# Kernel tuning notes

Hardware: AMD Instinct MI355X
Metric: run time of the kernel (lower is better)

The kernel has to match this reference:

```python
import jax, jax.numpy as jnp
import numpy as np

B, S, D, H = 16, 577, 768, 12  # batch, seq (24*24+1 cls), hidden, heads
WH, WW = 24, 24
HEAD = D // H
NUM_REL = (2 * WH - 1) * (2 * WW - 1) + 3  # 2212


def make_rel_pos_index(wh, ww):
    # mirrors TFData2VecVisionRelativePositionBias.get_position_index
    xx, yy = np.meshgrid(np.arange(wh), np.arange(ww))  # 'xy' indexing like tf.meshgrid
    coords = np.stack([yy, xx], axis=0).reshape(2, -1)  # [2, wh*ww]
    rel = coords[:, :, None] - coords[:, None, :]       # [2, N, N]
    rel = rel.transpose(1, 2, 0)                        # [N, N, 2]
    rx = (rel[:, :, 0] + wh - 1) * (2 * ww - 1)
    ry = rel[:, :, 1] + ww - 1
    idx = rx + ry                                       # [N, N]
    n = idx.shape[0]
    top = np.full((1, n), NUM_REL - 3, dtype=idx.dtype)
    left = np.full((n, 1), NUM_REL - 2, dtype=idx.dtype)
    corner = np.full((1, 1), NUM_REL - 1, dtype=idx.dtype)
    idx = np.concatenate([top, idx], axis=0)
    idx = np.concatenate([np.concatenate([corner, left], axis=0), idx], axis=1)
    return idx.astype(np.int32)  # [N+1, N+1]


def setup_inputs() -> dict:
    key = jax.random.key(0)
    ks = jax.random.split(key, 6)
    scale = 0.02
    return {
        "hidden_states": jax.random.normal(ks[0], (B, S, D), jnp.float32),
        "Wq": jax.random.normal(ks[1], (D, D), jnp.float32) * scale,
        "bq": jnp.zeros((D,), jnp.float32),
        "Wk": jax.random.normal(ks[2], (D, D), jnp.float32) * scale,
        "Wv": jax.random.normal(ks[3], (D, D), jnp.float32) * scale,
        "bv": jnp.zeros((D,), jnp.float32),
        "rel_pos_bias_table": jax.random.normal(ks[4], (NUM_REL, H), jnp.float32) * scale,
        "rel_pos_index": jnp.asarray(make_rel_pos_index(WH, WW)),
    }


def reference(hidden_states, Wq, bq, Wk, Wv, bv, rel_pos_bias_table, rel_pos_index):
    b, s, _ = hidden_states.shape
    q = (hidden_states @ Wq + bq).reshape(b, s, H, HEAD).transpose(0, 2, 1, 3)
    k = (hidden_states @ Wk).reshape(b, s, H, HEAD).transpose(0, 2, 1, 3)
    v = (hidden_states @ Wv + bv).reshape(b, s, H, HEAD).transpose(0, 2, 1, 3)
    scores = jnp.einsum("bhqd,bhkd->bhqk", q, k) / jnp.sqrt(jnp.float32(HEAD))
    # gathered relative position bias: [S, S, H] -> [H, S, S]
    bias = rel_pos_bias_table[rel_pos_index].transpose(2, 0, 1)
    scores = scores + bias[None]
    probs = jax.nn.softmax(scores, axis=-1)
    out = jnp.einsum("bhqk,bhkd->bhqd", probs, v)
    out = out.transpose(0, 2, 1, 3).reshape(b, s, D)
    return out
```

## Files before the change

### kernel.cpp

```cpp
#include <hip/hip_runtime.h>
#include <hip/hip_bf16.h>


typedef __attribute__((ext_vector_type(8))) short bf16x8;
typedef __attribute__((ext_vector_type(4))) float f32x4;
typedef unsigned short u16;

#define SEQ 577
#define MTOT 9232
#define QKV_STRIDE 7090176
#define VT_PITCH 640
#define B_PITCH 640

static __device__ __forceinline__ u16 f2bf(float x) {
  unsigned int u = __float_as_uint(x);
  u = (u + 0x7FFFu + ((u >> 16) & 1u)) >> 16;
  return (u16)u;
}
static __device__ __forceinline__ float bf2f(u16 v) {
  return __uint_as_float(((unsigned int)v) << 16);
}

static __device__ __forceinline__ void gload_lds16(const void* g, void* l) {
  __builtin_amdgcn_global_load_lds(
      (const __attribute__((address_space(1))) unsigned int*)g,
      (__attribute__((address_space(3))) unsigned int*)l, 16, 0, 0);
}

__global__ __launch_bounds__(256) void prep(
    const float* __restrict__ Wq, const float* __restrict__ Wk,
    const float* __restrict__ Wv, const float* __restrict__ X,
    u16* __restrict__ WT, u16* __restrict__ Xb) {
  const int bid = blockIdx.x;
  if (bid < 1728) {
    __shared__ float t[32][33];
    const int z = bid / 576;
    const int rem = bid - z * 576;
    const int kx = rem % 24, ny = rem / 24;
    const float* W = (z == 0) ? Wq : (z == 1) ? Wk : Wv;
    int x = threadIdx.x & 31;
    int y = threadIdx.x >> 5;
    int k0 = kx * 32;
    int n0 = ny * 32;
#pragma unroll
    for (int i = 0; i < 4; ++i)
      t[y + i * 8][x] = W[(size_t)(k0 + y + i * 8) * 768 + n0 + x];
    __syncthreads();
    u16* o = WT + (size_t)z * 589824;
#pragma unroll
    for (int i = 0; i < 4; ++i)
      o[(size_t)(n0 + y + i * 8) * 768 + k0 + x] = f2bf(t[x][y + i * 8]);
  } else {
    size_t i = ((size_t)(bid - 1728) * 256 + threadIdx.x) * 8;
    if (i >= (size_t)MTOT * 768) return;
    const float4* xp = (const float4*)(X + i);
    float4 a = xp[0], b = xp[1];
    u16 pk[8] = {f2bf(a.x), f2bf(a.y), f2bf(a.z), f2bf(a.w),
                 f2bf(b.x), f2bf(b.y), f2bf(b.z), f2bf(b.w)};
    *(int4*)(Xb + i) = *(const int4*)pk;
  }
}

__global__ __launch_bounds__(256) void prep2(
    const u16* __restrict__ v,
    u16* __restrict__ vT,
    const float* __restrict__ table, const int* __restrict__ idx,
    u16* __restrict__ biasm) {
  const int bid = blockIdx.x;
  const int tid = threadIdx.x;
  if (bid < 960) {
    const int tile = bid % 5;
    const int bh = bid / 5;
    const int b = bh / 12, h = bh % 12;
    __shared__ u16 T[128][64];
    const int s0 = tile * 128;
    const u16* vp = v + (size_t)b * SEQ * 768 + h * 64;
#pragma unroll
    for (int it = 0; it < 4; ++it) {
      int c = tid + it * 256;
      int r = c >> 3, ko = (c & 7) << 3;
      int gs = s0 + r;
      int4 val = make_int4(0, 0, 0, 0);
      if (gs < SEQ) val = *(const int4*)(vp + (size_t)gs * 768 + ko);
      *(int4*)&T[r][ko ^ (((r >> 3) & 7) << 3)] = val;
    }
    __syncthreads();
    u16* op = vT + (size_t)bh * 64 * VT_PITCH;
#pragma unroll
    for (int it = 0; it < 4; ++it) {
      int c = tid + it * 256;
      int d = c >> 4, so = (c & 15) << 3;
      u16 tmp[8];
#pragma unroll
      for (int j = 0; j < 8; ++j) {
        int rr = so + j;
        tmp[j] = T[rr][d ^ (((rr >> 3) & 7) << 3)];
      }
      *(int4*)(op + (size_t)d * VT_PITCH + s0 + so) = *(const int4*)tmp;
    }
  } else {
    const int r = bid - 960;
    const int q = r % 577;
    const int h = r / 577;
    for (int k = tid; k < B_PITCH; k += 256) {
      u16 vv = 0;
      if (k < SEQ) vv = f2bf(table[idx[q * SEQ + k] * 12 + h]);
      biasm[((size_t)h * SEQ + q) * B_PITCH + k] = vv;
    }
  }
}

__global__ __launch_bounds__(256) void qkv_gemm(
    const u16* __restrict__ Xb,
    const u16* __restrict__ WT,
    const float* __restrict__ bq, const float* __restrict__ bv,
    u16* __restrict__ qkv) {
  const int bid = blockIdx.x;
  const int xcd = bid & 7;
  const int local = bid >> 3;
  const int mp = (local / 18) * 8 + xcd;
  if (mp >= 73) return;
  const int nw = local % 18;
  const int widx = nw % 3;
  const int m0 = mp * 128;
  const int n0 = (nw / 3) * 128;

  const int tid = threadIdx.x;
  const int lane = tid & 63;
  const int w = tid >> 6;
  const int wm = (w >> 1) * 64;
  const int wn = (w & 1) * 64;
  const int quad = lane >> 4;
  const int l15 = lane & 15;

  __shared__ u16 SH[2][2][128][32];

  const u16* Wp = WT + (size_t)widx * 589824;

  const int srow = w * 32 + (lane >> 2);
  const int scol = (lane & 3) * 8;

  int r0 = m0 + srow;
  int r1 = r0 + 16;
  if (r0 > MTOT - 1) r0 = MTOT - 1;
  if (r1 > MTOT - 1) r1 = MTOT - 1;
  const u16* a0 = Xb + (size_t)r0 * 768 + scol;
  const u16* a1 = Xb + (size_t)r1 * 768 + scol;
  const u16* b0 = Wp + (size_t)(n0 + srow) * 768 + scol;
  const u16* b1 = Wp + (size_t)(n0 + srow + 16) * 768 + scol;

  f32x4 acc[4][4];
#pragma unroll
  for (int i = 0; i < 4; ++i)
#pragma unroll
    for (int j = 0; j < 4; ++j) acc[i][j] = (f32x4){0.f, 0.f, 0.f, 0.f};

  gload_lds16(a0, &SH[0][0][w * 32][0]);
  gload_lds16(a1, &SH[0][0][w * 32 + 16][0]);
  gload_lds16(b0, &SH[0][1][w * 32][0]);
  gload_lds16(b1, &SH[0][1][w * 32 + 16][0]);
  __syncthreads();

  for (int kt = 0; kt < 24; ++kt) {
    const int cur = kt & 1;
    if (kt < 23) {
      const int k1 = (kt + 1) * 32;
      const int nb = cur ^ 1;
      gload_lds16(a0 + k1, &SH[nb][0][w * 32][0]);
      gload_lds16(a1 + k1, &SH[nb][0][w * 32 + 16][0]);
      gload_lds16(b0 + k1, &SH[nb][1][w * 32][0]);
      gload_lds16(b1 + k1, &SH[nb][1][w * 32 + 16][0]);
    }
    bf16x8 af[4], bfv[4];
#pragma unroll
    for (int i = 0; i < 4; ++i)
      af[i] = *(const bf16x8*)(&SH[cur][0][wm + i * 16 + l15][quad * 8]);
#pragma unroll
    for (int i = 0; i < 4; ++i)
      bfv[i] = *(const bf16x8*)(&SH[cur][1][wn + i * 16 + l15][quad * 8]);
#pragma unroll
    for (int mt = 0; mt < 4; ++mt)
#pragma unroll
      for (int nt = 0; nt < 4; ++nt)
        acc[mt][nt] = __builtin_amdgcn_mfma_f32_16x16x32_bf16(af[mt], bfv[nt],
                                                              acc[mt][nt], 0, 0, 0);
    __syncthreads();
  }

  const float scale = (widx == 0) ? 0.125f : 1.0f;
  u16* ob = qkv + (size_t)widx * QKV_STRIDE;
  float biasv[4];
#pragma unroll
  for (int nt = 0; nt < 4; ++nt) {
    int n = n0 + wn + nt * 16 + l15;
    biasv[nt] = (widx == 0) ? bq[n] * 0.125f : (widx == 2) ? bv[n] : 0.f;
  }
  u16* S = &SH[0][0][0][0];
#pragma unroll
  for (int half = 0; half < 2; ++half) {
    if ((w >> 1) == half) {
#pragma unroll
      for (int mt = 0; mt < 4; ++mt)
#pragma unroll
        for (int nt = 0; nt < 4; ++nt)
#pragma unroll
          for (int r = 0; r < 4; ++r) {
            int rowl = mt * 16 + quad * 4 + r;
            int col = wn + nt * 16 + l15;
            int cs = (col + quad * 32) & 127;
            S[rowl * 128 + cs] = f2bf(acc[mt][nt][r] * scale + biasv[nt]);
          }
    }
    __syncthreads();
#pragma unroll
    for (int it = 0; it < 4; ++it) {
      int c = tid + it * 256;
      int rowl = c >> 4, ch = c & 15;
      int m = m0 + half * 64 + rowl;
      if (m < MTOT) {
        int cs = (ch * 8 + ((rowl >> 2) & 3) * 32) & 127;
        *(int4*)(ob + (size_t)m * 768 + n0 + ch * 8) = *(const int4*)&S[rowl * 128 + cs];
      }
    }
    __syncthreads();
  }
}

__global__ __launch_bounds__(512) void attn(
    const u16* __restrict__ qk, const u16* __restrict__ vT,
    const u16* __restrict__ biasm, float* __restrict__ out) {
  const int bh = blockIdx.x;
  const int qt = blockIdx.y;
  const int b = bh / 12, h = bh - b * 12;
  const int tid = threadIdx.x;
  const int lane = tid & 63;
  const int w = tid >> 6;
  const int quad = lane >> 4;
  const int l15 = lane & 15;

  const u16* qp = qk + (size_t)b * SEQ * 768 + h * 64;
  const u16* kp = qp + (size_t)QKV_STRIDE;
  const u16* vtp = vT + (size_t)bh * 64 * VT_PITCH;
  const u16* bp = biasm + (size_t)h * SEQ * B_PITCH;

  __shared__ u16 Ks[64][72];
  __shared__ u16 VTs[64][72];
  __shared__ u16 Ps[8][16][72];

  const int qrow0 = qt * 128 + w * 16;

  bf16x8 qf[2];
  {
    int row = qrow0 + l15;
    if (row > 576) row = 576;
    qf[0] = *(const bf16x8*)(qp + (size_t)row * 768 + quad * 8);
    qf[1] = *(const bf16x8*)(qp + (size_t)row * 768 + 32 + quad * 8);
  }
  int brow[4];
#pragma unroll
  for (int r = 0; r < 4; ++r) {
    int rr = qrow0 + quad * 4 + r;
    if (rr > 576) rr = 576;
    brow[r] = rr;
  }

  float lacc[4] = {0.f, 0.f, 0.f, 0.f};
  f32x4 O[4];
#pragma unroll
  for (int dt = 0; dt < 4; ++dt) O[dt] = (f32x4){0.f, 0.f, 0.f, 0.f};

  for (int kt = 0; kt < 10; ++kt) {
    const int kbase = kt * 64;
    u16 bb[4][4];
#pragma unroll
    for (int nt = 0; nt < 4; ++nt)
#pragma unroll
      for (int r = 0; r < 4; ++r)
        bb[nt][r] = bp[(size_t)brow[r] * B_PITCH + kbase + nt * 16 + l15];

    {
      int rr = tid >> 3, ko = (tid & 7) << 3;
      int gk = kbase + rr;
      int4 kvv = make_int4(0, 0, 0, 0);
      if (gk < SEQ) kvv = *(const int4*)(kp + (size_t)gk * 768 + ko);
      *(int4*)&Ks[rr][ko] = kvv;
      *(int4*)&VTs[rr][ko] = *(const int4*)(vtp + (size_t)rr * VT_PITCH + kbase + ko);
    }
    __syncthreads();

    f32x4 s[4];
#pragma unroll
    for (int nt = 0; nt < 4; ++nt) {
      f32x4 z = (f32x4){bf2f(bb[nt][0]), bf2f(bb[nt][1]),
                        bf2f(bb[nt][2]), bf2f(bb[nt][3])};
      bf16x8 kf0 = *(const bf16x8*)(&Ks[nt * 16 + l15][quad * 8]);
      bf16x8 kf1 = *(const bf16x8*)(&Ks[nt * 16 + l15][32 + quad * 8]);
      z = __builtin_amdgcn_mfma_f32_16x16x32_bf16(qf[0], kf0, z, 0, 0, 0);
      z = __builtin_amdgcn_mfma_f32_16x16x32_bf16(qf[1], kf1, z, 0, 0, 0);
      s[nt] = z;
    }

    const bool full = (kbase + 64 <= SEQ);
#pragma unroll
    for (int nt = 0; nt < 4; ++nt) {
#pragma unroll
      for (int r = 0; r < 4; ++r) {
        float p = __expf(s[nt][r]);
        unsigned int u = __float_as_uint(p);
        float pt = __uint_as_float(u & 0xFFFF0000u);
        if (full) lacc[r] += pt;
        else lacc[r] += ((kbase + nt * 16 + l15) < SEQ) ? pt : 0.f;
        Ps[w][quad * 4 + r][((nt ^ quad) << 4) + l15] = (u16)(u >> 16);
      }
    }

#pragma unroll
    for (int ks = 0; ks < 2; ++ks) {
      int cc = (ks * 32 + quad * 8) ^ ((l15 >> 2) << 4);
      bf16x8 pf = *(const bf16x8*)(&Ps[w][l15][cc]);
#pragma unroll
      for (int dt = 0; dt < 4; ++dt) {
        bf16x8 vf = *(const bf16x8*)(&VTs[dt * 16 + l15][ks * 32 + quad * 8]);
        O[dt] = __builtin_amdgcn_mfma_f32_16x16x32_bf16(pf, vf, O[dt], 0, 0, 0);
      }
    }
    __syncthreads();
  }

#pragma unroll
  for (int r = 0; r < 4; ++r) {
    float l = lacc[r];
    l += __shfl_xor(l, 1);
    l += __shfl_xor(l, 2);
    l += __shfl_xor(l, 4);
    l += __shfl_xor(l, 8);
    int row = qrow0 + quad * 4 + r;
    if (row < SEQ) {
      float inv = 1.f / l;
#pragma unroll
      for (int dt = 0; dt < 4; ++dt)
        out[((size_t)(b * SEQ + row)) * 768 + h * 64 + dt * 16 + l15] = O[dt][r] * inv;
    }
  }
}

extern "C" void kernel_launch(void* const* d_in, const int* in_sizes, int n_in,
                              void* d_out, int out_size, void* d_ws, size_t ws_size,
                              hipStream_t stream) {
  const float* hs = (const float*)d_in[0];
  const float* Wq = (const float*)d_in[1];
  const float* bq = (const float*)d_in[2];
  const float* Wk = (const float*)d_in[3];
  const float* Wv = (const float*)d_in[4];
  const float* bv = (const float*)d_in[5];
  const float* table = (const float*)d_in[6];
  const int* idx = (const int*)d_in[7];
  float* out = (float*)d_out;

  char* ws = (char*)d_ws;
  u16* qkv = (u16*)ws;
  u16* WT = (u16*)(ws + 42541056);
  u16* Xb = (u16*)(ws + 46080000);
  u16* vT = (u16*)(ws + 42541056);
  u16* biasm = (u16*)(ws + 58269696);

  hipLaunchKernelGGL(prep, dim3(5190), dim3(256), 0, stream, Wq, Wk, Wv, hs, WT, Xb);
  hipLaunchKernelGGL(qkv_gemm, dim3(1440), dim3(256), 0, stream, Xb, WT, bq, bv, qkv);
  hipLaunchKernelGGL(prep2, dim3(7884), dim3(256), 0, stream,
                     qkv + 2 * (size_t)QKV_STRIDE, vT, table, idx, biasm);
  hipLaunchKernelGGL(attn, dim3(192, 5), dim3(512), 0, stream, qkv, vT, biasm, out);
}
```

Measured before the change: 208.5 us.

## Enlarge QKV GEMM tiles with triple-buffered LDS and prefetch attention operands

The QKV GEMM moves from 128x128 tiles with 256 threads and double buffering to 256x384 tiles with 512 threads. It adds triple-buffered direct-to-LDS loads, XOR-swizzled LDS layout, explicit waitcnt/barrier scheduling and MFMA priority raising. The aim is more operand reuse per block and less LDS and global traffic per FLOP. The relative-position bias matrix is stored transposed (key-major), so each lane loads four consecutive query biases as one short4 instead of four scalar loads. The attention loop also register-prefetches the next K, V^T and bias tiles to overlap global loads with compute. The cost is higher register pressure and only 240 GEMM blocks, which may underfill the GPU.

After: 223.6 us. +7.3%, slower.

```diff
diff --git a/kernel.cpp b/kernel.cpp
--- a/kernel.cpp
+++ b/kernel.cpp
@@ -10,7 +10,8 @@
 #define MTOT 9232
 #define QKV_STRIDE 7090176
 #define VT_PITCH 640
-#define B_PITCH 640
+#define BT_K 584
+#define BT_Q 632
 
 static __device__ __forceinline__ u16 f2bf(float x) {
   unsigned int u = __float_as_uint(x);
@@ -65,7 +66,7 @@
     const u16* __restrict__ v,
     u16* __restrict__ vT,
     const float* __restrict__ table, const int* __restrict__ idx,
-    u16* __restrict__ biasm) {
+    u16* __restrict__ biasT) {
   const int bid = blockIdx.x;
   const int tid = threadIdx.x;
   if (bid < 960) {
@@ -100,126 +101,166 @@
     }
   } else {
     const int r = bid - 960;
-    const int q = r % 577;
-    const int h = r / 577;
-    for (int k = tid; k < B_PITCH; k += 256) {
+    const int k = r % BT_K;
+    const int h = r / BT_K;
+    u16* op = biasT + ((size_t)h * BT_K + k) * BT_Q;
+    for (int q = tid; q < BT_Q; q += 256) {
       u16 vv = 0;
-      if (k < SEQ) vv = f2bf(table[idx[q * SEQ + k] * 12 + h]);
-      biasm[((size_t)h * SEQ + q) * B_PITCH + k] = vv;
-    }
-  }
-}
-
-__global__ __launch_bounds__(256) void qkv_gemm(
+      if (q < SEQ && k < SEQ) vv = f2bf(table[idx[q * SEQ + k] * 12 + h]);
+      op[q] = vv;
+    }
+  }
+}
+
+#define G_STAGE_A(BS, KT, U)                                                   \
+  gload_lds16(aptr[(U)] + (KT) * 32, &SAB[(BS)][((U) * 128 + w16) * 32])
+#define G_STAGE_B(BS, KT, U)                                                   \
+  gload_lds16(bptr + (size_t)(U) * 128 * 768 + (KT) * 32,                      \
+              &SAB[(BS)][8192 + ((U) * 128 + w16) * 32])
+
+__global__ __launch_bounds__(512, 2) void qkv_gemm(
     const u16* __restrict__ Xb,
     const u16* __restrict__ WT,
     const float* __restrict__ bq, const float* __restrict__ bv,
     u16* __restrict__ qkv) {
   const int bid = blockIdx.x;
-  const int xcd = bid & 7;
-  const int local = bid >> 3;
-  const int mp = (local / 18) * 8 + xcd;
-  if (mp >= 73) return;
-  const int nw = local % 18;
-  const int widx = nw % 3;
-  const int m0 = mp * 128;
-  const int n0 = (nw / 3) * 128;
+  const int x = bid & 7;
+  const int l = bid >> 3;
+  const int mt = x + 8 * (l / 6);
+  if (mt >= 37) return;
+  const int nt = l % 6;
+  const int m0 = mt * 256;
+  const int widx = nt >> 1;
+  const int nb = (nt & 1) * 384;
 
   const int tid = threadIdx.x;
   const int lane = tid & 63;
   const int w = tid >> 6;
-  const int wm = (w >> 1) * 64;
-  const int wn = (w & 1) * 64;
+  const int wm2 = w >> 2;
+  const int wn = w & 3;
   const int quad = lane >> 4;
   const int l15 = lane & 15;
-
-  __shared__ u16 SH[2][2][128][32];
-
-  const u16* Wp = WT + (size_t)widx * 589824;
-
-  const int srow = w * 32 + (lane >> 2);
-  const int scol = (lane & 3) * 8;
-
-  int r0 = m0 + srow;
-  int r1 = r0 + 16;
-  if (r0 > MTOT - 1) r0 = MTOT - 1;
-  if (r1 > MTOT - 1) r1 = MTOT - 1;
-  const u16* a0 = Xb + (size_t)r0 * 768 + scol;
-  const u16* a1 = Xb + (size_t)r1 * 768 + scol;
-  const u16* b0 = Wp + (size_t)(n0 + srow) * 768 + scol;
-  const u16* b1 = Wp + (size_t)(n0 + srow + 16) * 768 + scol;
-
-  f32x4 acc[4][4];
-#pragma unroll
-  for (int i = 0; i < 4; ++i)
-#pragma unroll
-    for (int j = 0; j < 4; ++j) acc[i][j] = (f32x4){0.f, 0.f, 0.f, 0.f};
-
-  gload_lds16(a0, &SH[0][0][w * 32][0]);
-  gload_lds16(a1, &SH[0][0][w * 32 + 16][0]);
-  gload_lds16(b0, &SH[0][1][w * 32][0]);
-  gload_lds16(b1, &SH[0][1][w * 32 + 16][0]);
-  __syncthreads();
-
-  for (int kt = 0; kt < 24; ++kt) {
-    const int cur = kt & 1;
-    if (kt < 23) {
-      const int k1 = (kt + 1) * 32;
-      const int nb = cur ^ 1;
-      gload_lds16(a0 + k1, &SH[nb][0][w * 32][0]);
-      gload_lds16(a1 + k1, &SH[nb][0][w * 32 + 16][0]);
-      gload_lds16(b0 + k1, &SH[nb][1][w * 32][0]);
-      gload_lds16(b1 + k1, &SH[nb][1][w * 32 + 16][0]);
-    }
-    bf16x8 af[4], bfv[4];
+  const int w16 = w * 16;
+
+  __shared__ u16 SAB[3][20480];
+
+  const int srow = w16 + (lane >> 2);
+  const int ce8 = (((lane & 3) ^ ((lane >> 3) & 3))) * 8;
+  const u16* aptr[2];
+#pragma unroll
+  for (int u = 0; u < 2; ++u) {
+    int rr = m0 + u * 128 + srow;
+    if (rr > MTOT - 1) rr = MTOT - 1;
+    aptr[u] = Xb + (size_t)rr * 768 + ce8;
+  }
+  const u16* bptr =
+      WT + (size_t)widx * 589824 + (size_t)(nb + srow) * 768 + ce8;
+
+  const int ca8 = (quad ^ ((l15 >> 1) & 3)) * 8;
+
+  f32x4 acc[8][6];
+#pragma unroll
+  for (int i = 0; i < 8; ++i)
+#pragma unroll
+    for (int j = 0; j < 6; ++j) acc[i][j] = (f32x4){0.f, 0.f, 0.f, 0.f};
+  bf16x8 af[4], bfr[6];
+
+  G_STAGE_A(0, 0, 0); G_STAGE_A(0, 0, 1);
+  G_STAGE_B(0, 0, 0); G_STAGE_B(0, 0, 1); G_STAGE_B(0, 0, 2);
+  G_STAGE_A(1, 1, 0); G_STAGE_A(1, 1, 1);
+  G_STAGE_B(1, 1, 0); G_STAGE_B(1, 1, 1); G_STAGE_B(1, 1, 2);
+  asm volatile("s_waitcnt vmcnt(5)" ::: "memory");
+  __builtin_amdgcn_s_barrier();
+  asm volatile("" ::: "memory");
+
+  int bs = 0, bt2 = 2;
+  for (int t = 0; t < 24; ++t) {
 #pragma unroll
     for (int i = 0; i < 4; ++i)
-      af[i] = *(const bf16x8*)(&SH[cur][0][wm + i * 16 + l15][quad * 8]);
+      af[i] = *(const bf16x8*)&SAB[bs][(wm2 * 128 + i * 16 + l15) * 32 + ca8];
+#pragma unroll
+    for (int j = 0; j < 6; ++j)
+      bfr[j] = *(const bf16x8*)&SAB[bs][8192 + (wn * 96 + j * 16 + l15) * 32 + ca8];
+    if (t <= 21) { G_STAGE_A(bt2, t + 2, 0); G_STAGE_A(bt2, t + 2, 1); G_STAGE_B(bt2, t + 2, 0); }
+    asm volatile("" ::: "memory");
+    __builtin_amdgcn_s_barrier();
+    asm volatile("s_waitcnt lgkmcnt(0)" ::: "memory");
+    __builtin_amdgcn_s_setprio(1);
+#pragma unroll
+    for (int j = 0; j < 6; ++j)
+#pragma unroll
+      for (int i = 0; i < 4; ++i)
+        acc[i][j] = __builtin_amdgcn_mfma_f32_16x16x32_bf16(af[i], bfr[j],
+                                                            acc[i][j], 0, 0, 0);
+    __builtin_amdgcn_s_setprio(0);
+    asm volatile("" ::: "memory");
+    __builtin_amdgcn_s_barrier();
+    asm volatile("" ::: "memory");
 #pragma unroll
     for (int i = 0; i < 4; ++i)
-      bfv[i] = *(const bf16x8*)(&SH[cur][1][wn + i * 16 + l15][quad * 8]);
-#pragma unroll
-    for (int mt = 0; mt < 4; ++mt)
-#pragma unroll
-      for (int nt = 0; nt < 4; ++nt)
-        acc[mt][nt] = __builtin_amdgcn_mfma_f32_16x16x32_bf16(af[mt], bfv[nt],
-                                                              acc[mt][nt], 0, 0, 0);
-    __syncthreads();
+      af[i] = *(const bf16x8*)&SAB[bs][(wm2 * 128 + 64 + i * 16 + l15) * 32 + ca8];
+#pragma unroll
+    for (int j = 0; j < 6; ++j)
+      bfr[j] = *(const bf16x8*)&SAB[bs][8192 + (wn * 96 + j * 16 + l15) * 32 + ca8];
+    if (t <= 21) { G_STAGE_B(bt2, t + 2, 1); G_STAGE_B(bt2, t + 2, 2); }
+    asm volatile("" ::: "memory");
+    __builtin_amdgcn_s_barrier();
+    asm volatile("s_waitcnt lgkmcnt(0)" ::: "memory");
+    __builtin_amdgcn_s_setprio(1);
+#pragma unroll
+    for (int j = 0; j < 6; ++j)
+#pragma unroll
+      for (int i = 0; i < 4; ++i)
+        acc[4 + i][j] = __builtin_amdgcn_mfma_f32_16x16x32_bf16(
+            af[i], bfr[j], acc[4 + i][j], 0, 0, 0);
+    __builtin_amdgcn_s_setprio(0);
+    if (t < 22) {
+      asm volatile("s_waitcnt vmcnt(5)" ::: "memory");
+    } else if (t == 22) {
+      asm volatile("s_waitcnt vmcnt(0)" ::: "memory");
+    }
+    asm volatile("" ::: "memory");
+    __builtin_amdgcn_s_barrier();
+    asm volatile("" ::: "memory");
+    bs = (bs == 2) ? 0 : bs + 1;
+    bt2 = (bt2 == 2) ? 0 : bt2 + 1;
   }
 
   const float scale = (widx == 0) ? 0.125f : 1.0f;
-  u16* ob = qkv + (size_t)widx * QKV_STRIDE;
-  float biasv[4];
-#pragma unroll
-  for (int nt = 0; nt < 4; ++nt) {
-    int n = n0 + wn + nt * 16 + l15;
-    biasv[nt] = (widx == 0) ? bq[n] * 0.125f : (widx == 2) ? bv[n] : 0.f;
-  }
-  u16* S = &SH[0][0][0][0];
+  float biasv[6];
+#pragma unroll
+  for (int nf = 0; nf < 6; ++nf) {
+    int n = nb + wn * 96 + nf * 16 + l15;
+    biasv[nf] = (widx == 0) ? bq[n] * 0.125f : (widx == 2) ? bv[n] : 0.f;
+  }
+  u16* E = &SAB[0][0];
+  u16* ob = qkv + (size_t)widx * QKV_STRIDE + nb;
 #pragma unroll
   for (int half = 0; half < 2; ++half) {
-    if ((w >> 1) == half) {
-#pragma unroll
-      for (int mt = 0; mt < 4; ++mt)
-#pragma unroll
-        for (int nt = 0; nt < 4; ++nt)
+    if (wm2 == half) {
+#pragma unroll
+      for (int mf = 0; mf < 8; ++mf)
+#pragma unroll
+        for (int nf = 0; nf < 6; ++nf)
 #pragma unroll
           for (int r = 0; r < 4; ++r) {
-            int rowl = mt * 16 + quad * 4 + r;
-            int col = wn + nt * 16 + l15;
-            int cs = (col + quad * 32) & 127;
-            S[rowl * 128 + cs] = f2bf(acc[mt][nt][r] * scale + biasv[nt]);
+            int rowl = mf * 16 + quad * 4 + r;
+            int col = wn * 96 + nf * 16 + l15;
+            int colr = (((col >> 4) ^ quad) << 4) | (col & 15);
+            E[rowl * 384 + colr] = f2bf(acc[mf][nf][r] * scale + biasv[nf]);
           }
     }
     __syncthreads();
-#pragma unroll
-    for (int it = 0; it < 4; ++it) {
-      int c = tid + it * 256;
-      int rowl = c >> 4, ch = c & 15;
-      int m = m0 + half * 64 + rowl;
+#pragma unroll 4
+    for (int it = 0; it < 12; ++it) {
+      int c = it * 512 + tid;
+      int row = c / 48;
+      int ch = c - row * 48;
+      int m = m0 + half * 128 + row;
       if (m < MTOT) {
-        int cs = (ch * 8 + ((rowl >> 2) & 3) * 32) & 127;
-        *(int4*)(ob + (size_t)m * 768 + n0 + ch * 8) = *(const int4*)&S[rowl * 128 + cs];
+        int g = (ch >> 1) ^ ((row >> 2) & 3);
+        int colr = (g << 4) + (ch & 1) * 8;
+        *(int4*)(ob + (size_t)m * 768 + ch * 8) = *(const int4*)&E[row * 384 + colr];
       }
     }
     __syncthreads();
@@ -228,7 +269,7 @@
 
 __global__ __launch_bounds__(512) void attn(
     const u16* __restrict__ qk, const u16* __restrict__ vT,
-    const u16* __restrict__ biasm, float* __restrict__ out) {
+    const u16* __restrict__ biasT, float* __restrict__ out) {
   const int bh = blockIdx.x;
   const int qt = blockIdx.y;
   const int b = bh / 12, h = bh - b * 12;
@@ -241,7 +282,7 @@
   const u16* qp = qk + (size_t)b * SEQ * 768 + h * 64;
   const u16* kp = qp + (size_t)QKV_STRIDE;
   const u16* vtp = vT + (size_t)bh * 64 * VT_PITCH;
-  const u16* bp = biasm + (size_t)h * SEQ * B_PITCH;
+  const u16* btp = biasT + (size_t)h * BT_K * BT_Q;
 
   __shared__ u16 Ks[64][72];
   __shared__ u16 VTs[64][72];
@@ -256,43 +297,61 @@
     qf[0] = *(const bf16x8*)(qp + (size_t)row * 768 + quad * 8);
     qf[1] = *(const bf16x8*)(qp + (size_t)row * 768 + 32 + quad * 8);
   }
-  int brow[4];
-#pragma unroll
-  for (int r = 0; r < 4; ++r) {
-    int rr = qrow0 + quad * 4 + r;
-    if (rr > 576) rr = 576;
-    brow[r] = rr;
-  }
+  int qb = qrow0 + quad * 4;
+  if (qb > 576) qb = 576;
+
+  const int rr = tid >> 3, ko = (tid & 7) << 3;
 
   float lacc[4] = {0.f, 0.f, 0.f, 0.f};
   f32x4 O[4];
 #pragma unroll
   for (int dt = 0; dt < 4; ++dt) O[dt] = (f32x4){0.f, 0.f, 0.f, 0.f};
 
+  int4 pk_k, pk_v;
+  short4 pb[4];
+  {
+    int gk = rr;
+    pk_k = make_int4(0, 0, 0, 0);
+    if (gk < SEQ) pk_k = *(const int4*)(kp + (size_t)gk * 768 + ko);
+    pk_v = *(const int4*)(vtp + (size_t)rr * VT_PITCH + ko);
+#pragma unroll
+    for (int nt = 0; nt < 4; ++nt) {
+      int kb = nt * 16 + l15;
+      if (kb > 576) kb = 576;
+      pb[nt] = *(const short4*)(btp + (size_t)kb * BT_Q + qb);
+    }
+  }
+
   for (int kt = 0; kt < 10; ++kt) {
     const int kbase = kt * 64;
-    u16 bb[4][4];
+    *(int4*)&Ks[rr][ko] = pk_k;
+    *(int4*)&VTs[rr][ko] = pk_v;
+    __syncthreads();
+
+    f32x4 zz[4];
 #pragma unroll
     for (int nt = 0; nt < 4; ++nt)
-#pragma unroll
-      for (int r = 0; r < 4; ++r)
-        bb[nt][r] = bp[(size_t)brow[r] * B_PITCH + kbase + nt * 16 + l15];
-
-    {
-      int rr = tid >> 3, ko = (tid & 7) << 3;
-      int gk = kbase + rr;
-      int4 kvv = make_int4(0, 0, 0, 0);
-      if (gk < SEQ) kvv = *(const int4*)(kp + (size_t)gk * 768 + ko);
-      *(int4*)&Ks[rr][ko] = kvv;
-      *(int4*)&VTs[rr][ko] = *(const int4*)(vtp + (size_t)rr * VT_PITCH + kbase + ko);
-    }
-    __syncthreads();
+      zz[nt] = (f32x4){bf2f((u16)pb[nt].x), bf2f((u16)pb[nt].y),
+                       bf2f((u16)pb[nt].z), bf2f((u16)pb[nt].w)};
+
+    if (kt < 9) {
+      const int nk = kbase + 64;
+      int gk = nk + rr;
+      pk_k = make_int4(0, 0, 0, 0);
+      if (gk < SEQ) pk_k = *(const int4*)(kp + (size_t)gk * 768 + ko);
+      pk_v = *(const int4*)(vtp + (size_t)rr * VT_PITCH + nk + ko);
+#pragma unroll
+      for (int nt = 0; nt < 4; ++nt) {
+        int kb = nk + nt * 16 + l15;
+        if (kb > 576) kb = 576;
+        pb[nt] = *(const short4*)(btp + (size_t)kb * BT_Q + qb);
+      }
+    }
 
     f32x4 s[4];
 #pragma unroll
     for (int nt = 0; nt < 4; ++nt) {
-      f32x4 z = (f32x4){bf2f(bb[nt][0]), bf2f(bb[nt][1]),
-                        bf2f(bb[nt][2]), bf2f(bb[nt][3])};
+      f32x4 z = zz[nt];
       bf16x8 kf0 = *(const bf16x8*)(&Ks[nt * 16 + l15][quad * 8]);
       bf16x8 kf1 = *(const bf16x8*)(&Ks[nt * 16 + l15][32 + quad * 8]);
       z = __builtin_amdgcn_mfma_f32_16x16x32_bf16(qf[0], kf0, z, 0, 0, 0);
@@ -362,11 +421,11 @@
   u16* WT = (u16*)(ws + 42541056);
   u16* Xb = (u16*)(ws + 46080000);
   u16* vT = (u16*)(ws + 42541056);
-  u16* biasm = (u16*)(ws + 58269696);
+  u16* biasT = (u16*)(ws + 58269696);
 
   hipLaunchKernelGGL(prep, dim3(5190), dim3(256), 0, stream, Wq, Wk, Wv, hs, WT, Xb);
-  hipLaunchKernelGGL(qkv_gemm, dim3(1440), dim3(256), 0, stream, Xb, WT, bq, bv, qkv);
-  hipLaunchKernelGGL(prep2, dim3(7884), dim3(256), 0, stream,
-                     qkv + 2 * (size_t)QKV_STRIDE, vT, table, idx, biasm);
-  hipLaunchKernelGGL(attn, dim3(192, 5), dim3(512), 0, stream, qkv, vT, biasm, out);
-}
+  hipLaunchKernelGGL(qkv_gemm, dim3(240), dim3(512), 0, stream, Xb, WT, bq, bv, qkv);
+  hipLaunchKernelGGL(prep2, dim3(7968), dim3(256), 0, stream,
+                     qkv + 2 * (size_t)QKV_STRIDE, vT, table, idx, biasT);
+  hipLaunchKernelGGL(attn, dim3(192, 5), dim3(512), 0, stream, qkv, vT, biasT, out);
+}
```
